# Optimization experiments

Hardware: AMD Instinct MI355X
Metric: run time of the kernel (lower is better)

## Reference

```python
import jax, jax.numpy as jnp
import numpy as np

SIX = 6
CONNECT_RANDN_K = 0.01
SIGMOID_K = 1
KERNAL_D = 128
INPUTS_D = 64
KERNAL_A = 3
STRIDE = 1
BATCH = 16
HW = 32


def _build_pq_table():
    # [2*SIX, 64]: row j (j<6) selects log(x_j) when bit j of i is 1,
    # row j+6 selects log(1-x_j) when bit j is 0 (bit order = MSB first, as in the torch code)
    t = np.zeros((2 * SIX, 2 ** SIX), np.float32)
    for i in range(2 ** SIX):
        bins = format(i, '06b')
        for j in range(SIX):
            if bins[j] == '0':
                t[j + SIX, i] = 1.0
            else:
                t[j, i] = 1.0
    return jnp.asarray(t)


def _build_appointed():
    # buffer: +6 bias on one random input channel of every group's first sub-kernel
    rng = np.random.RandomState(0)
    a = np.zeros((KERNAL_D * SIX, INPUTS_D, KERNAL_A, KERNAL_A), np.float32)
    for i in range(KERNAL_D):
        r = rng.randint(0, INPUTS_D)
        a[i * SIX, r, :, :] += 6.0
    return jnp.asarray(a)


def _lut_init():
    lut = np.zeros((KERNAL_D, 2 ** SIX), np.float32)
    for i in range(2 ** SIX):
        a = format(i, '06b').count('0') / float(SIX)
        if a == 0.0:
            a = 0.01
        if a == 1.0:
            a = 0.99
        lut[:, i] = np.log(a / (1.0 - a))
    return jnp.asarray(lut)


P_Q_TABLE = _build_pq_table()
APPOINTED = _build_appointed()


def setup_inputs() -> dict:
    key = jax.random.key(0)
    k1, k2 = jax.random.split(key)
    inputs = jax.random.uniform(k1, (BATCH, INPUTS_D, HW, HW), dtype=jnp.float32)
    connect_kernal = jax.random.normal(
        k2, (KERNAL_D * SIX, INPUTS_D, KERNAL_A, KERNAL_A), dtype=jnp.float32) * CONNECT_RANDN_K
    lut = _lut_init()
    return {"inputs": inputs, "connect_kernal": connect_kernal, "lut": lut}


def _forward(inputs, connect_kernal, lut):
    # argmax-derived one-hot kernel (the branch actually taken in the source)
    ck = connect_kernal / CONNECT_RANDN_K + APPOINTED
    flat = ck.reshape(KERNAL_D * SIX, -1)
    one_hot = jax.nn.one_hot(jnp.argmax(flat, axis=-1), flat.shape[-1], dtype=inputs.dtype)
    kern = one_hot.reshape(ck.shape)  # [kd*6, in_d, ka, ka]

    x = jax.lax.conv_general_dilated(
        inputs, kern, window_strides=(STRIDE, STRIDE), padding='VALID',
        dimension_numbers=('NCHW', 'OIHW', 'NCHW'))  # [B, kd*6, H', W']
    B, _, Ho, Wo = x.shape
    x = x.transpose(0, 2, 3, 1).reshape(-1, KERNAL_D, SIX)  # [N, kd, 6]

    # LutLayer (train path): p_q = [1-x, x], relu+eps, log, matmul LUT table, exp, weight by lut
    eps = 1e-7
    p_q = jax.nn.relu(jnp.concatenate([1.0 - x, x], axis=-1)) + eps  # [N, kd, 12]
    lut_p = jnp.exp(jnp.einsum('ndk,kt->ndt', jnp.log(p_q), P_Q_TABLE))  # [N, kd, 64]
    y = jnp.sum(lut_p * lut, axis=-1)  # [N, kd]

    y = y.reshape(B, Ho, Wo, KERNAL_D).transpose(0, 3, 1, 2)  # NCHW

    # BatchNorm2d(affine=False), training mode: biased batch stats
    mean = y.mean(axis=(0, 2, 3), keepdims=True)
    var = y.var(axis=(0, 2, 3), keepdims=True)
    y = (y - mean) / jnp.sqrt(var + 1e-5)

    nk, uk = jax.random.split(jax.random.key(42))
    y = y + jax.random.normal(nk, y.shape, y.dtype) * 0.2
    x_norm = y
    s = jax.nn.sigmoid(y * SIGMOID_K)
    r = jax.random.uniform(uk, y.shape, y.dtype)
    x_quant = (s > r).astype(y.dtype)
    return x_norm, x_quant


def reference(inputs, connect_kernal, lut):
    return _forward(inputs, connect_kernal, lut)
```

## Files before the change

### kernel.cpp

```cpp
#include <hip/hip_runtime.h>
#include <stdint.h>

#define NELEM 1843200
#define NPIX  1048576

typedef float v2f __attribute__((ext_vector_type(2)));

struct RselT { uint32_t v[128]; };
constexpr RselT compute_rsel(){
  uint32_t mt[624] = {};
  mt[0] = 0u;
  for (int i=1;i<624;i++) mt[i] = 1812433253u * (mt[i-1] ^ (mt[i-1] >> 30)) + (uint32_t)i;
  for (int i=0;i<624;i++){
    uint32_t y = (mt[i] & 0x80000000u) | (mt[(i+1)%624] & 0x7fffffffu);
    uint32_t v = mt[(i+397)%624] ^ (y >> 1);
    if (y & 1u) v ^= 0x9908b0dfu;
    mt[i] = v;
  }
  RselT r{};
  for (int k=0;k<128;k++){
    uint32_t z = mt[k];
    z ^= z >> 11;
    z ^= (z << 7)  & 0x9d2c5680u;
    z ^= (z << 15) & 0xefc60000u;
    z ^= z >> 18;
    r.v[k] = z & 63u;
  }
  return r;
}
__device__ __constant__ RselT RSEL = compute_rsel();

__device__ __forceinline__ uint32_t rotl32(uint32_t x, uint32_t r){ return (x<<r)|(x>>(32u-r)); }

__device__ __forceinline__ void tf2x32(uint32_t k0, uint32_t k1, uint32_t& x0, uint32_t& x1){
  uint32_t ks0=k0, ks1=k1, ks2=k0^k1^0x1BD11BDAu;
  x0 += ks0; x1 += ks1;
#define TFR(r) { x0 += x1; x1 = rotl32(x1,(r)); x1 ^= x0; }
  TFR(13) TFR(15) TFR(26) TFR(6)
  x0 += ks1; x1 += ks2 + 1u;
  TFR(17) TFR(29) TFR(16) TFR(24)
  x0 += ks2; x1 += ks0 + 2u;
  TFR(13) TFR(15) TFR(26) TFR(6)
  x0 += ks0; x1 += ks1 + 3u;
  TFR(17) TFR(29) TFR(16) TFR(24)
  x0 += ks1; x1 += ks2 + 4u;
  TFR(13) TFR(15) TFR(26) TFR(6)
  x0 += ks2; x1 += ks0 + 5u;
#undef TFR
}

struct K2 { uint32_t a, b; };
constexpr uint32_t rotl_c(uint32_t x, int r){ return (x<<r)|(x>>(32-r)); }
constexpr K2 tf_c(uint32_t k0, uint32_t k1, uint32_t x0, uint32_t x1){
  uint32_t ks0=k0, ks1=k1, ks2=k0^k1^0x1BD11BDAu;
  x0 += ks0; x1 += ks1;
#define TFC(r) { x0 += x1; x1 = rotl_c(x1,(r)); x1 ^= x0; }
  TFC(13) TFC(15) TFC(26) TFC(6)
  x0 += ks1; x1 += ks2 + 1u;
  TFC(17) TFC(29) TFC(16) TFC(24)
  x0 += ks2; x1 += ks0 + 2u;
  TFC(13) TFC(15) TFC(26) TFC(6)
  x0 += ks0; x1 += ks1 + 3u;
  TFC(17) TFC(29) TFC(16) TFC(24)
  x0 += ks1; x1 += ks2 + 4u;
  TFC(13) TFC(15) TFC(26) TFC(6)
  x0 += ks2; x1 += ks0 + 5u;
#undef TFC
  return K2{x0, x1};
}
constexpr K2 NK = tf_c(0u, 42u, 0u, 0u);
constexpr K2 UK = tf_c(0u, 42u, 0u, 1u);

__device__ __forceinline__ float exp2_raw(float x){
#if __has_builtin(__builtin_amdgcn_exp2f)
  return __builtin_amdgcn_exp2f(x);
#else
  float r; asm("v_exp_f32 %0, %1" : "=v"(r) : "v"(x)); return r;
#endif
}

__device__ __forceinline__ float exp_exact(float a){
#pragma clang fp contract(off)
  const float C  = 0x1.715476p+0f;
  const float CC = 0x1.4ae0bep-26f;
  float ph = a * C;
  float pl = fmaf(a, CC, fmaf(a, C, -ph));
  float e  = __builtin_rintf(ph);
  float A  = (ph - e) + pl;
  return __builtin_ldexpf(exp2_raw(A), (int)e);
}

__global__ __launch_bounds__(64) void argmax_k(const float* __restrict__ ck,
    uint32_t* __restrict__ sel, double* __restrict__ Sz){
  int o = blockIdx.x;
  int lane = threadIdx.x;
  if (o == 0){
    #pragma unroll
    for (int q=0;q<4;q++) Sz[lane*4+q] = 0.0;
  }
  uint32_t rb = RSEL.v[o/6];
  bool isap = (o % 6) == 0;
  float bv = -3.4e38f; int bi = 0x7fffffff;
  for (int t = lane; t < 576; t += 64){
    float v = ck[o*576 + t] / 0.01f;
    if (isap && (uint32_t)(t/9) == rb) v += 6.0f;
    if (v > bv) { bv = v; bi = t; }
  }
  for (int off=32; off>0; off>>=1){
    float ov = __shfl_xor(bv, off);
    int   oi = __shfl_xor(bi, off);
    if (ov > bv || (ov == bv && oi < bi)) { bv = ov; bi = oi; }
  }
  if (lane == 0) sel[o] = (uint32_t)bi;
}

__global__ __launch_bounds__(256) void pre_k(const float* __restrict__ inp,
                                             v2f* __restrict__ lg){
  int i = blockIdx.x * 256 + threadIdx.x;
  float x = inp[i];
  v2f r;
  r[0] = logf(x + 1e-7f);
  r[1] = logf((1.0f - x) + 1e-7f);
  lg[i] = r;
}

template<int PRE>
__global__ __launch_bounds__(256) void c1_k(const float* __restrict__ inp,
    const v2f* __restrict__ lg,
    const float* __restrict__ lut, const uint32_t* __restrict__ sel,
    float* __restrict__ yraw, double* __restrict__ S1, double* __restrict__ S2){
#pragma clang fp contract(off)
  const int blk = blockIdx.x;
  const int b = blk >> 7;
  const int d = blk & 127;
  int off6[6];
  #pragma unroll
  for (int j=0;j<6;j++){
    uint32_t t = sel[d*6+j];
    int cc = (int)(t/9u); int rem = (int)(t%9u);
    off6[j] = cc*1024 + (rem/3)*32 + (rem%3);
  }
  const int pbase = b*65536;
  const float* w = lut + d*64;
  double acc1 = 0.0, acc2 = 0.0;
  #pragma unroll 1
  for (int p = threadIdx.x; p < 900; p += 256){
    int ho = p/30, wo = p - ho*30;
    int pix = pbase + ho*32 + wo;
    float lx[6], l1x[6];
    #pragma unroll
    for (int j=0;j<6;j++){
      if (PRE){
        v2f v = lg[pix + off6[j]];
        lx[j] = v[0]; l1x[j] = v[1];
      } else {
        float x = inp[pix + off6[j]];
        lx[j]  = logf(x + 1e-7f);
        l1x[j] = logf((1.0f - x) + 1e-7f);
      }
    }
    float S5[32];
    S5[0] = 0.0f;
    #pragma unroll
    for (int k=1;k<32;k++){
      const int m = 2*k;
      S5[k] = S5[(m & (m-1)) >> 1] + l1x[5 - __builtin_ctz((unsigned)m)];
    }
    float y = 0.0f;
    #pragma unroll
    for (int k=0;k<32;k++){
      const int m = 2*k;
      float a0 = S5[k];
      float a1 = S5[k] + l1x[5];
      #pragma unroll
      for (int j=0;j<5;j++){
        if (!(m & (32 >> j))){ a0 = a0 + lx[j]; a1 = a1 + lx[j]; }
      }
      a0 = a0 + lx[5];
      float t0 = exp_exact(a0) * w[m];
      float t1 = exp_exact(a1) * w[m+1];
      y = y + t0;
      y = y + t1;
    }
    yraw[blk*900 + p] = y;
    acc1 += (double)y;
    acc2 += (double)y * (double)y;
  }
  #pragma unroll
  for (int off=32; off>0; off>>=1){
    acc1 += __shfl_down(acc1, off);
    acc2 += __shfl_down(acc2, off);
  }
  __shared__ double sh1[4], sh2[4];
  int wid = threadIdx.x >> 6;
  if ((threadIdx.x & 63) == 0){ sh1[wid] = acc1; sh2[wid] = acc2; }
  __syncthreads();
  if (threadIdx.x == 0){
    atomicAdd(&S1[d], sh1[0]+sh1[1]+sh1[2]+sh1[3]);
    atomicAdd(&S2[d], sh2[0]+sh2[1]+sh2[2]+sh2[3]);
  }
}

__device__ __forceinline__ float erfinv_xla(float x){
#pragma clang fp contract(off)
  float w = -log1pf(-(x*x));
  float p;
  if (w < 5.0f){
    w = w - 2.5f;
    p = 2.81022636e-08f;
    p = 3.43273939e-07f  + p*w;
    p = -3.5233877e-06f  + p*w;
    p = -4.39150654e-06f + p*w;
    p = 0.00021858087f   + p*w;
    p = -0.00125372503f  + p*w;
    p = -0.00417768164f  + p*w;
    p = 0.246640727f     + p*w;
    p = 1.50140941f      + p*w;
  } else {
    w = sqrtf(w) - 3.0f;
    p = -0.000200214257f;
    p = 0.000100950558f  + p*w;
    p = 0.00134934322f   + p*w;
    p = -0.00367342844f  + p*w;
    p = 0.00573950773f   + p*w;
    p = -0.0076224613f   + p*w;
    p = 0.00943887047f   + p*w;
    p = 1.00167406f      + p*w;
    p = 2.83297682f      + p*w;
  }
  return p * x;
}

__device__ __forceinline__ float fast_tanh_xla(float x){
  float ax = fabsf(x);
  float cx = fmaxf(fminf(x, 7.90531110763549805f), -7.90531110763549805f);
  float x2 = cx*cx;
  float np_ = fmaf(x2, -2.76076847742355e-16f, 2.00018790482477e-13f);
  np_ = fmaf(x2, np_, -8.60467152213735e-11f);
  np_ = fmaf(x2, np_, 5.12229709037114e-08f);
  np_ = fmaf(x2, np_, 1.48572235717979e-05f);
  np_ = fmaf(x2, np_, 6.37261928875436e-04f);
  np_ = fmaf(x2, np_, 4.89352455891786e-03f);
  float num = cx * np_;
  float dp_ = fmaf(x2, 1.19825839466702e-06f, 1.18534705686654e-04f);
  dp_ = fmaf(x2, dp_, 2.26843463243900e-03f);
  dp_ = fmaf(x2, dp_, 4.89352518554385e-03f);
  return (ax < 0.0004f) ? x : (num / dp_);
}

__global__ __launch_bounds__(256) void c3_k(float* __restrict__ out,
    const double* __restrict__ S1, const double* __restrict__ S2){
#pragma clang fp contract(off)
  const int base = blockIdx.x * 256;
  __shared__ float smv[4];
  const int dA = (base / 900) & 127;
  const int dB = ((base + 255) / 900) & 127;
  if (threadIdx.x < 2){
    int dd = threadIdx.x ? dB : dA;
    double m = S1[dd] / 14400.0;
    float m32 = (float)m;
    double ey2 = S2[dd] / 14400.0;
    double v = ey2 - 2.0*(double)m32*m + (double)m32*(double)m32;
    smv[threadIdx.x*2+0] = m32;
    smv[threadIdx.x*2+1] = (float)v;
  }
  __syncthreads();
  const int i = base + threadIdx.x;
  const int d = (i / 900) & 127;
  const int sb = (d != dA) ? 2 : 0;
  const float m32 = smv[sb], var32 = smv[sb+1];

  float yr = out[NELEM + i];
  float y = (yr - m32) / sqrtf(var32 + 1e-5f);

  { uint32_t x0 = 0u, x1 = (uint32_t)i; tf2x32(NK.a, NK.b, x0, x1);
    uint32_t nb = x0 ^ x1;
    float u01 = __uint_as_float((nb >> 9) | 0x3f800000u) - 1.0f;
    const float lo = __uint_as_float(0xBF7FFFFFu);
    float un = u01 * 2.0f + lo;
    un = fmaxf(lo, un);
    float noise = __uint_as_float(0x3FB504F3u) * erfinv_xla(un);
    y = y + noise * 0.2f;
  }
  out[i] = y;

  uint32_t x0 = 0u, x1 = (uint32_t)i;
  tf2x32(UK.a, UK.b, x0, x1);
  uint32_t rb = x0 ^ x1;
  float r = __uint_as_float((rb >> 9) | 0x3f800000u) - 1.0f;

  float s = 0.5f + 0.5f * fast_tanh_xla(0.5f * y);
  out[NELEM + i] = (s > r) ? 1.0f : 0.0f;
}

extern "C" void kernel_launch(void* const* d_in, const int* in_sizes, int n_in,
                              void* d_out, int out_size, void* d_ws, size_t ws_size,
                              hipStream_t stream) {
  (void)in_sizes; (void)n_in; (void)out_size;
  const float* inp = (const float*)d_in[0];
  const float* ck  = (const float*)d_in[1];
  const float* lut = (const float*)d_in[2];
  float* out = (float*)d_out;

  uint32_t* sel = (uint32_t*)d_ws;
  double*   S1  = (double*)((char*)d_ws + 4096);
  double*   S2  = S1 + 128;
  v2f*      lg  = (v2f*)((char*)d_ws + 8192);

  const size_t ws_need = 8192 + (size_t)NPIX * 8;

  hipLaunchKernelGGL(argmax_k, dim3(768),  dim3(64),  0, stream, ck, sel, S1);
  if (ws_size >= ws_need){
    hipLaunchKernelGGL(pre_k,   dim3(NPIX/256), dim3(256), 0, stream, inp, lg);
    hipLaunchKernelGGL(c1_k<1>, dim3(2048),     dim3(256), 0, stream, inp, lg, lut, sel, out + NELEM, S1, S2);
  } else {
    hipLaunchKernelGGL(c1_k<0>, dim3(2048),     dim3(256), 0, stream, inp, lg, lut, sel, out + NELEM, S1, S2);
  }
  hipLaunchKernelGGL(c3_k, dim3(7200), dim3(256), 0, stream, out, S1, S2);
}
```

Baseline: 80.24 us.

## Fuse all stages into one persistent kernel with software grid barriers

Replaces the four separate launches (argmax, log precompute, LUT compute, normalize/noise) with a single persistent kernel of 512 blocks. Software grid barriers built on atomics separate the phases, and the LUT outputs stay in shared memory between phases, so the intermediate y buffer no longer goes through global memory. This removes launch gaps and a global round trip. In exchange, all 512 blocks must be co-resident for the spin barrier to work, and the per-block parallelism of the compute phase becomes coarser.

```diff
diff --git a/kernel.cpp b/kernel.cpp
--- a/kernel.cpp
+++ b/kernel.cpp
@@ -3,6 +3,7 @@
 
 #define NELEM 1843200
 #define NPIX  1048576
+#define GRID  512
 
 typedef float v2f __attribute__((ext_vector_type(2)));
 
@@ -88,117 +89,6 @@
   float e  = __builtin_rintf(ph);
   float A  = (ph - e) + pl;
   return __builtin_ldexpf(exp2_raw(A), (int)e);
-}
-
-__global__ __launch_bounds__(64) void argmax_k(const float* __restrict__ ck,
-    uint32_t* __restrict__ sel, double* __restrict__ Sz){
-  int o = blockIdx.x;
-  int lane = threadIdx.x;
-  if (o == 0){
-    #pragma unroll
-    for (int q=0;q<4;q++) Sz[lane*4+q] = 0.0;
-  }
-  uint32_t rb = RSEL.v[o/6];
-  bool isap = (o % 6) == 0;
-  float bv = -3.4e38f; int bi = 0x7fffffff;
-  for (int t = lane; t < 576; t += 64){
-    float v = ck[o*576 + t] / 0.01f;
-    if (isap && (uint32_t)(t/9) == rb) v += 6.0f;
-    if (v > bv) { bv = v; bi = t; }
-  }
-  for (int off=32; off>0; off>>=1){
-    float ov = __shfl_xor(bv, off);
-    int   oi = __shfl_xor(bi, off);
-    if (ov > bv || (ov == bv && oi < bi)) { bv = ov; bi = oi; }
-  }
-  if (lane == 0) sel[o] = (uint32_t)bi;
-}
-
-__global__ __launch_bounds__(256) void pre_k(const float* __restrict__ inp,
-                                             v2f* __restrict__ lg){
-  int i = blockIdx.x * 256 + threadIdx.x;
-  float x = inp[i];
-  v2f r;
-  r[0] = logf(x + 1e-7f);
-  r[1] = logf((1.0f - x) + 1e-7f);
-  lg[i] = r;
-}
-
-template<int PRE>
-__global__ __launch_bounds__(256) void c1_k(const float* __restrict__ inp,
-    const v2f* __restrict__ lg,
-    const float* __restrict__ lut, const uint32_t* __restrict__ sel,
-    float* __restrict__ yraw, double* __restrict__ S1, double* __restrict__ S2){
-#pragma clang fp contract(off)
-  const int blk = blockIdx.x;
-  const int b = blk >> 7;
-  const int d = blk & 127;
-  int off6[6];
-  #pragma unroll
-  for (int j=0;j<6;j++){
-    uint32_t t = sel[d*6+j];
-    int cc = (int)(t/9u); int rem = (int)(t%9u);
-    off6[j] = cc*1024 + (rem/3)*32 + (rem%3);
-  }
-  const int pbase = b*65536;
-  const float* w = lut + d*64;
-  double acc1 = 0.0, acc2 = 0.0;
-  #pragma unroll 1
-  for (int p = threadIdx.x; p < 900; p += 256){
-    int ho = p/30, wo = p - ho*30;
-    int pix = pbase + ho*32 + wo;
-    float lx[6], l1x[6];
-    #pragma unroll
-    for (int j=0;j<6;j++){
-      if (PRE){
-        v2f v = lg[pix + off6[j]];
-        lx[j] = v[0]; l1x[j] = v[1];
-      } else {
-        float x = inp[pix + off6[j]];
-        lx[j]  = logf(x + 1e-7f);
-        l1x[j] = logf((1.0f - x) + 1e-7f);
-      }
-    }
-    float S5[32];
-    S5[0] = 0.0f;
-    #pragma unroll
-    for (int k=1;k<32;k++){
-      const int m = 2*k;
-      S5[k] = S5[(m & (m-1)) >> 1] + l1x[5 - __builtin_ctz((unsigned)m)];
-    }
-    float y = 0.0f;
-    #pragma unroll
-    for (int k=0;k<32;k++){
-      const int m = 2*k;
-      float a0 = S5[k];
-      float a1 = S5[k] + l1x[5];
-      #pragma unroll
-      for (int j=0;j<5;j++){
-        if (!(m & (32 >> j))){ a0 = a0 + lx[j]; a1 = a1 + lx[j]; }
-      }
-      a0 = a0 + lx[5];
-      float t0 = exp_exact(a0) * w[m];
-      float t1 = exp_exact(a1) * w[m+1];
-      y = y + t0;
-      y = y + t1;
-    }
-    yraw[blk*900 + p] = y;
-    acc1 += (double)y;
-    acc2 += (double)y * (double)y;
-  }
-  #pragma unroll
-  for (int off=32; off>0; off>>=1){
-    acc1 += __shfl_down(acc1, off);
-    acc2 += __shfl_down(acc2, off);
-  }
-  __shared__ double sh1[4], sh2[4];
-  int wid = threadIdx.x >> 6;
-  if ((threadIdx.x & 63) == 0){ sh1[wid] = acc1; sh2[wid] = acc2; }
-  __syncthreads();
-  if (threadIdx.x == 0){
-    atomicAdd(&S1[d], sh1[0]+sh1[1]+sh1[2]+sh1[3]);
-    atomicAdd(&S2[d], sh2[0]+sh2[1]+sh2[2]+sh2[3]);
-  }
 }
 
 __device__ __forceinline__ float erfinv_xla(float x){
@@ -248,6 +138,271 @@
   return (ax < 0.0004f) ? x : (num / dp_);
 }
 
+__device__ __forceinline__ void grid_bar(unsigned* cnt){
+  __syncthreads();
+  if (threadIdx.x == 0){
+    __threadfence();
+    unsigned t = atomicAdd(cnt, 1u);
+    unsigned target = (t/GRID + 1u)*GRID;
+    while (atomicAdd(cnt, 0u) < target) { __builtin_amdgcn_s_sleep(2); }
+    __threadfence();
+  }
+  __syncthreads();
+}
+
+__global__ __launch_bounds__(256, 4) void fused_k(
+    const float* __restrict__ inp, const float* __restrict__ ck,
+    const float* __restrict__ lut, float* __restrict__ out,
+    v2f* __restrict__ lg, uint32_t* __restrict__ sel,
+    double* __restrict__ S1, double* __restrict__ S2,
+    unsigned* __restrict__ cnt)
+{
+#pragma clang fp contract(off)
+  const int blk = blockIdx.x;
+  const int tid = threadIdx.x;
+  __shared__ double sh1[4], sh2[4];
+  __shared__ float smv[8];
+  __shared__ float yl[3600];
+
+  #pragma unroll
+  for (int q=0;q<8;q++){
+    int i = blk*2048 + q*256 + tid;
+    float x = inp[i];
+    v2f r;
+    r[0] = logf(x + 1e-7f);
+    r[1] = logf((1.0f - x) + 1e-7f);
+    lg[i] = r;
+  }
+  {
+    int wv = tid >> 6, lane = tid & 63;
+    int c = blk + 512*wv;
+    if (wv < 2 && c < 768){
+      uint32_t rb = RSEL.v[c/6];
+      bool isap = (c % 6) == 0;
+      float bv = -3.4e38f; int bi = 0x7fffffff;
+      for (int t = lane; t < 576; t += 64){
+        float v = ck[c*576 + t] / 0.01f;
+        if (isap && (uint32_t)(t/9) == rb) v += 6.0f;
+        if (v > bv) { bv = v; bi = t; }
+      }
+      for (int off=32; off>0; off>>=1){
+        float ov = __shfl_xor(bv, off);
+        int   oi = __shfl_xor(bi, off);
+        if (ov > bv || (ov == bv && oi < bi)) { bv = ov; bi = oi; }
+      }
+      if (lane == 0) sel[c] = (uint32_t)bi;
+    }
+  }
+  if (blk == 511) ((double*)S1)[tid] = 0.0;
+
+  grid_bar(cnt);
+
+  #pragma unroll 1
+  for (int sb=0; sb<4; ++sb){
+    const int pair = blk*4 + sb;
+    const int b = pair >> 7;
+    const int d = pair & 127;
+    int off6[6];
+    #pragma unroll
+    for (int j=0;j<6;j++){
+      uint32_t t = sel[d*6+j];
+      int cc = (int)(t/9u); int rem = (int)(t%9u);
+      off6[j] = cc*1024 + (rem/3)*32 + (rem%3);
+    }
+    const int pbase = b*65536;
+    const float* w = lut + d*64;
+    double acc1 = 0.0, acc2 = 0.0;
+    #pragma unroll 1
+    for (int q=0;q<4;q++){
+      const int p = tid + q*256;
+      if (p < 900){
+        int ho = p/30, wo = p - ho*30;
+        int pix = pbase + ho*32 + wo;
+        float lx[6], l1x[6];
+        #pragma unroll
+        for (int j=0;j<6;j++){
+          v2f v = lg[pix + off6[j]];
+          lx[j] = v[0]; l1x[j] = v[1];
+        }
+        float S5[32];
+        S5[0] = 0.0f;
+        #pragma unroll
+        for (int k=1;k<32;k++){
+          const int m = 2*k;
+          S5[k] = S5[(m & (m-1)) >> 1] + l1x[5 - __builtin_ctz((unsigned)m)];
+        }
+        float y = 0.0f;
+        #pragma unroll
+        for (int k=0;k<32;k++){
+          const int m = 2*k;
+          float a0 = S5[k];
+          float a1 = S5[k] + l1x[5];
+          #pragma unroll
+          for (int j=0;j<5;j++){
+            if (!(m & (32 >> j))){ a0 = a0 + lx[j]; a1 = a1 + lx[j]; }
+          }
+          a0 = a0 + lx[5];
+          float t0 = exp_exact(a0) * w[m];
+          float t1 = exp_exact(a1) * w[m+1];
+          y = y + t0;
+          y = y + t1;
+        }
+        yl[sb*900 + p] = y;
+        acc1 += (double)y;
+        acc2 += (double)y * (double)y;
+      }
+    }
+    #pragma unroll
+    for (int off=32; off>0; off>>=1){
+      acc1 += __shfl_down(acc1, off);
+      acc2 += __shfl_down(acc2, off);
+    }
+    int wid = tid >> 6;
+    if ((tid & 63) == 0){ sh1[wid] = acc1; sh2[wid] = acc2; }
+    __syncthreads();
+    if (tid == 0){
+      atomicAdd(&S1[d], sh1[0]+sh1[1]+sh1[2]+sh1[3]);
+      atomicAdd(&S2[d], sh2[0]+sh2[1]+sh2[2]+sh2[3]);
+    }
+    __syncthreads();
+  }
+
+  grid_bar(cnt);
+
+  if (tid < 4){
+    const int dd = (blk*4 + tid) & 127;
+    double m = S1[dd] / 14400.0;
+    float m32 = (float)m;
+    double ey2 = S2[dd] / 14400.0;
+    double v = ey2 - 2.0*(double)m32*m + (double)m32*(double)m32;
+    smv[tid*2+0] = m32;
+    smv[tid*2+1] = (float)v;
+  }
+  __syncthreads();
+  #pragma unroll 1
+  for (int sb=0; sb<4; ++sb){
+    const int pair = blk*4 + sb;
+    const float m32 = smv[sb*2+0], var32 = smv[sb*2+1];
+    #pragma unroll 1
+    for (int q=0;q<4;q++){
+      const int p = tid + q*256;
+      if (p >= 900) continue;
+      const int i = pair*900 + p;
+      float y = (yl[sb*900 + p] - m32) / sqrtf(var32 + 1e-5f);
+      { uint32_t x0 = 0u, x1 = (uint32_t)i; tf2x32(NK.a, NK.b, x0, x1);
+        uint32_t nb = x0 ^ x1;
+        float u01 = __uint_as_float((nb >> 9) | 0x3f800000u) - 1.0f;
+        const float lo = __uint_as_float(0xBF7FFFFFu);
+        float un = u01 * 2.0f + lo;
+        un = fmaxf(lo, un);
+        float noise = __uint_as_float(0x3FB504F3u) * erfinv_xla(un);
+        y = y + noise * 0.2f;
+      }
+      out[i] = y;
+      uint32_t x0 = 0u, x1 = (uint32_t)i;
+      tf2x32(UK.a, UK.b, x0, x1);
+      uint32_t rb = x0 ^ x1;
+      float r = __uint_as_float((rb >> 9) | 0x3f800000u) - 1.0f;
+      float s = 0.5f + 0.5f * fast_tanh_xla(0.5f * y);
+      out[NELEM + i] = (s > r) ? 1.0f : 0.0f;
+    }
+  }
+}
+
+__global__ __launch_bounds__(64) void argmax_k(const float* __restrict__ ck,
+    uint32_t* __restrict__ sel, double* __restrict__ Sz){
+  int o = blockIdx.x;
+  int lane = threadIdx.x;
+  if (o == 0){
+    #pragma unroll
+    for (int q=0;q<4;q++) Sz[lane*4+q] = 0.0;
+  }
+  uint32_t rb = RSEL.v[o/6];
+  bool isap = (o % 6) == 0;
+  float bv = -3.4e38f; int bi = 0x7fffffff;
+  for (int t = lane; t < 576; t += 64){
+    float v = ck[o*576 + t] / 0.01f;
+    if (isap && (uint32_t)(t/9) == rb) v += 6.0f;
+    if (v > bv) { bv = v; bi = t; }
+  }
+  for (int off=32; off>0; off>>=1){
+    float ov = __shfl_xor(bv, off);
+    int   oi = __shfl_xor(bi, off);
+    if (ov > bv || (ov == bv && oi < bi)) { bv = ov; bi = oi; }
+  }
+  if (lane == 0) sel[o] = (uint32_t)bi;
+}
+
+__global__ __launch_bounds__(256) void c1_k(const float* __restrict__ inp,
+    const float* __restrict__ lut, const uint32_t* __restrict__ sel,
+    float* __restrict__ yraw, double* __restrict__ S1, double* __restrict__ S2){
+#pragma clang fp contract(off)
+  const int blk = blockIdx.x;
+  const int b = blk >> 7;
+  const int d = blk & 127;
+  int off6[6];
+  #pragma unroll
+  for (int j=0;j<6;j++){
+    uint32_t t = sel[d*6+j];
+    int cc = (int)(t/9u); int rem = (int)(t%9u);
+    off6[j] = cc*1024 + (rem/3)*32 + (rem%3);
+  }
+  const int pbase = b*65536;
+  const float* w = lut + d*64;
+  double acc1 = 0.0, acc2 = 0.0;
+  #pragma unroll 1
+  for (int p = threadIdx.x; p < 900; p += 256){
+    int ho = p/30, wo = p - ho*30;
+    int pix = pbase + ho*32 + wo;
+    float lx[6], l1x[6];
+    #pragma unroll
+    for (int j=0;j<6;j++){
+      float x = inp[pix + off6[j]];
+      lx[j]  = logf(x + 1e-7f);
+      l1x[j] = logf((1.0f - x) + 1e-7f);
+    }
+    float S5[32];
+    S5[0] = 0.0f;
+    #pragma unroll
+    for (int k=1;k<32;k++){
+      const int m = 2*k;
+      S5[k] = S5[(m & (m-1)) >> 1] + l1x[5 - __builtin_ctz((unsigned)m)];
+    }
+    float y = 0.0f;
+    #pragma unroll
+    for (int k=0;k<32;k++){
+      const int m = 2*k;
+      float a0 = S5[k];
+      float a1 = S5[k] + l1x[5];
+      #pragma unroll
+      for (int j=0;j<5;j++){
+        if (!(m & (32 >> j))){ a0 = a0 + lx[j]; a1 = a1 + lx[j]; }
+      }
+      a0 = a0 + lx[5];
+      float t0 = exp_exact(a0) * w[m];
+      float t1 = exp_exact(a1) * w[m+1];
+      y = y + t0;
+      y = y + t1;
+    }
+    yraw[blk*900 + p] = y;
+    acc1 += (double)y;
+    acc2 += (double)y * (double)y;
+  }
+  #pragma unroll
+  for (int off=32; off>0; off>>=1){
+    acc1 += __shfl_down(acc1, off);
+    acc2 += __shfl_down(acc2, off);
+  }
+  __shared__ double sh1[4], sh2[4];
+  int wid = threadIdx.x >> 6;
+  if ((threadIdx.x & 63) == 0){ sh1[wid] = acc1; sh2[wid] = acc2; }
+  __syncthreads();
+  if (threadIdx.x == 0){
+    atomicAdd(&S1[d], sh1[0]+sh1[1]+sh1[2]+sh1[3]);
+    atomicAdd(&S2[d], sh2[0]+sh2[1]+sh2[2]+sh2[3]);
+  }
+}
+
 __global__ __launch_bounds__(256) void c3_k(float* __restrict__ out,
     const double* __restrict__ S1, const double* __restrict__ S2){
 #pragma clang fp contract(off)
@@ -303,18 +458,20 @@
   float* out = (float*)d_out;
 
   uint32_t* sel = (uint32_t*)d_ws;
+  unsigned* cnt = (unsigned*)((char*)d_ws + 3072);
   double*   S1  = (double*)((char*)d_ws + 4096);
   double*   S2  = S1 + 128;
   v2f*      lg  = (v2f*)((char*)d_ws + 8192);
 
   const size_t ws_need = 8192 + (size_t)NPIX * 8;
 
-  hipLaunchKernelGGL(argmax_k, dim3(768),  dim3(64),  0, stream, ck, sel, S1);
   if (ws_size >= ws_need){
-    hipLaunchKernelGGL(pre_k,   dim3(NPIX/256), dim3(256), 0, stream, inp, lg);
-    hipLaunchKernelGGL(c1_k<1>, dim3(2048),     dim3(256), 0, stream, inp, lg, lut, sel, out + NELEM, S1, S2);
+    hipMemsetAsync(cnt, 0, 4, stream);
+    hipLaunchKernelGGL(fused_k, dim3(GRID), dim3(256), 0, stream,
+                       inp, ck, lut, out, lg, sel, S1, S2, cnt);
   } else {
-    hipLaunchKernelGGL(c1_k<0>, dim3(2048),     dim3(256), 0, stream, inp, lg, lut, sel, out + NELEM, S1, S2);
-  }
-  hipLaunchKernelGGL(c3_k, dim3(7200), dim3(256), 0, stream, out, S1, S2);
-}
+    hipLaunchKernelGGL(argmax_k, dim3(768),  dim3(64),  0, stream, ck, sel, S1);
+    hipLaunchKernelGGL(c1_k,     dim3(2048), dim3(256), 0, stream, inp, lut, sel, out + NELEM, S1, S2);
+    hipLaunchKernelGGL(c3_k,     dim3(7200), dim3(256), 0, stream, out, S1, S2);
+  }
+}
```

Result: slower. 166.3 us (+107.3%).
